# Kernel tuning notes

Measured on AMD Instinct MI355X. Metric: run time of the kernel, lower is better.

Reference implementation:

```python
import jax, jax.numpy as jnp
import numpy as np

B, S, H, NH = 4, 2048, 512, 8
HD = H // NH

def setup_inputs() -> dict:
    key = jax.random.key(0)
    ks = jax.random.split(key, 11)
    s = 1.0 / np.sqrt(H)
    return {
        "query": jax.random.normal(ks[0], (B, S, H), jnp.float32),
        "key_in": jax.random.normal(ks[1], (B, S, H), jnp.float32),
        "value": jax.random.normal(ks[2], (B, S, H), jnp.float32),
        "Wq": jax.random.uniform(ks[3], (H, H), jnp.float32, -s, s),
        "bq": jax.random.uniform(ks[4], (H,), jnp.float32, -s, s),
        "Wk": jax.random.uniform(ks[5], (H, H), jnp.float32, -s, s),
        "bk": jax.random.uniform(ks[6], (H,), jnp.float32, -s, s),
        "Wv": jax.random.uniform(ks[7], (H, H), jnp.float32, -s, s),
        "bv": jax.random.uniform(ks[8], (H,), jnp.float32, -s, s),
        "Wo": jax.random.uniform(ks[9], (H, H), jnp.float32, -s, s),
        "bo": jax.random.uniform(ks[10], (H,), jnp.float32, -s, s),
    }

def reference(query, key_in, value, Wq, bq, Wk, bk, Wv, bv, Wo, bo):
    scale = HD ** -0.5
    # projections; torch Linear: x @ W.T + b
    Q = (query @ Wq.T + bq).reshape(B, S, NH, HD).transpose(0, 2, 1, 3)   # [B,NH,S,HD]
    K = (key_in @ Wk.T + bk).reshape(B, S, NH, HD).transpose(0, 2, 1, 3)
    V = (value @ Wv.T + bv).reshape(B, S, NH, HD).transpose(0, 2, 1, 3)
    scores = jnp.einsum('bhqd,bhkd->bhqk', Q, K) * scale                  # [B,NH,S,S]
    attention = jax.nn.softmax(scores, axis=-1)                           # dropout in eval mode -> identity
    context = jnp.einsum('bhqk,bhkd->bhqd', attention, V)                 # [B,NH,S,HD]
    context = context.transpose(0, 2, 1, 3).reshape(B, S, H)
    output = context @ Wo.T + bo
    return (output, attention)
```

## Files before the change

kernel.cpp:

```cpp
#include <hip/hip_runtime.h>
#include <cstddef>

constexpr int kB  = 4;
constexpr int kS  = 2048;
constexpr int kH  = 512;
constexpr int kNH = 8;
constexpr int kHD = 64;
constexpr int kM  = kB * kS;
constexpr int kK  = 512;

#define FMA16(a, b)                                                        \
  do {                                                                     \
    acc[0][0] += a.x * b.x; acc[0][1] += a.x * b.y;                        \
    acc[0][2] += a.x * b.z; acc[0][3] += a.x * b.w;                        \
    acc[1][0] += a.y * b.x; acc[1][1] += a.y * b.y;                        \
    acc[1][2] += a.y * b.z; acc[1][3] += a.y * b.w;                        \
    acc[2][0] += a.z * b.x; acc[2][1] += a.z * b.y;                        \
    acc[2][2] += a.z * b.z; acc[2][3] += a.z * b.w;                        \
    acc[3][0] += a.w * b.x; acc[3][1] += a.w * b.y;                        \
    acc[3][2] += a.w * b.z; acc[3][3] += a.w * b.w;                        \
  } while (0)

template <int MODE>
__global__ __launch_bounds__(256) void gemm_nt_bias(
    const float* __restrict__ A, const float* __restrict__ W,
    const float* __restrict__ bias, float* __restrict__ out)
{
  __shared__ __align__(16) float As[16][68];
  __shared__ __align__(16) float Ws[16][68];

  const int tid  = threadIdx.x;
  const int ty   = tid >> 4;
  const int tx   = tid & 15;
  const int m0   = blockIdx.x * 64;
  const int n0   = blockIdx.y * 64;
  const int lrow = tid >> 2;
  const int lcol = (tid & 3) << 2;

  float acc[4][4] = {};

  for (int k0 = 0; k0 < kK; k0 += 16) {
    float4 av = *(const float4*)(A + (size_t)(m0 + lrow) * kK + k0 + lcol);
    float4 wv = *(const float4*)(W + (size_t)(n0 + lrow) * kK + k0 + lcol);
    __syncthreads();
    As[lcol + 0][lrow] = av.x; As[lcol + 1][lrow] = av.y;
    As[lcol + 2][lrow] = av.z; As[lcol + 3][lrow] = av.w;
    Ws[lcol + 0][lrow] = wv.x; Ws[lcol + 1][lrow] = wv.y;
    Ws[lcol + 2][lrow] = wv.z; Ws[lcol + 3][lrow] = wv.w;
    __syncthreads();
#pragma unroll
    for (int kk = 0; kk < 16; ++kk) {
      float4 a = *(const float4*)&As[kk][ty << 2];
      float4 b = *(const float4*)&Ws[kk][tx << 2];
      FMA16(a, b);
    }
  }

  float4 bv = *(const float4*)(bias + n0 + (tx << 2));
#pragma unroll
  for (int i = 0; i < 4; ++i) {
    const int m = m0 + (ty << 2) + i;
    float4 o = make_float4(acc[i][0] + bv.x, acc[i][1] + bv.y,
                           acc[i][2] + bv.z, acc[i][3] + bv.w);
    if (MODE == 0) {
      const int b = m >> 11;
      const int s = m & (kS - 1);
      const int h = n0 >> 6;
      const size_t idx =
          (((size_t)(b * kNH + h)) * kS + s) * kHD + (tx << 2);
      *(float4*)(out + idx) = o;
    } else {
      *(float4*)(out + (size_t)m * kH + n0 + (tx << 2)) = o;
    }
  }
}

__global__ __launch_bounds__(256) void scores_kernel(
    const float* __restrict__ Q, const float* __restrict__ Kh,
    float* __restrict__ attn)
{
  __shared__ __align__(16) float Qs[64][68];
  __shared__ __align__(16) float Ks[64][68];

  const int tid = threadIdx.x;
  const int ty  = tid >> 4;
  const int tx  = tid & 15;
  const int i0  = blockIdx.x * 64;
  const int j0  = blockIdx.y * 64;
  const int bh  = blockIdx.z;

  const float* Qb = Q  + (size_t)bh * kS * kHD;
  const float* Kb = Kh + (size_t)bh * kS * kHD;

#pragma unroll
  for (int it = 0; it < 4; ++it) {
    const int t   = tid + it * 256;
    const int row = t >> 4;
    const int c4  = (t & 15) << 2;
    float4 q  = *(const float4*)(Qb + (size_t)(i0 + row) * kHD + c4);
    float4 kv = *(const float4*)(Kb + (size_t)(j0 + row) * kHD + c4);
    Qs[c4 + 0][row] = q.x;  Qs[c4 + 1][row] = q.y;
    Qs[c4 + 2][row] = q.z;  Qs[c4 + 3][row] = q.w;
    Ks[c4 + 0][row] = kv.x; Ks[c4 + 1][row] = kv.y;
    Ks[c4 + 2][row] = kv.z; Ks[c4 + 3][row] = kv.w;
  }
  __syncthreads();

  float acc[4][4] = {};
#pragma unroll 8
  for (int kk = 0; kk < 64; ++kk) {
    float4 a = *(const float4*)&Qs[kk][ty << 2];
    float4 b = *(const float4*)&Ks[kk][tx << 2];
    FMA16(a, b);
  }

  const float scale = 0.125f;
#pragma unroll
  for (int i = 0; i < 4; ++i) {
    const size_t ridx =
        ((size_t)bh * kS + i0 + (ty << 2) + i) * kS + j0 + (tx << 2);
    *(float4*)(attn + ridx) = make_float4(acc[i][0] * scale, acc[i][1] * scale,
                                          acc[i][2] * scale, acc[i][3] * scale);
  }
}

__global__ __launch_bounds__(256) void softmax_kernel(float* __restrict__ attn)
{
  float* p = attn + (size_t)blockIdx.x * kS;
  const int tid = threadIdx.x;

  float4 v0 = ((const float4*)p)[tid];
  float4 v1 = ((const float4*)p)[tid + 256];

  float m = fmaxf(fmaxf(fmaxf(v0.x, v0.y), fmaxf(v0.z, v0.w)),
                  fmaxf(fmaxf(v1.x, v1.y), fmaxf(v1.z, v1.w)));
#pragma unroll
  for (int o = 32; o > 0; o >>= 1) m = fmaxf(m, __shfl_xor(m, o));

  __shared__ float redm[4];
  __shared__ float reds[4];
  const int w = tid >> 6;
  if ((tid & 63) == 0) redm[w] = m;
  __syncthreads();
  m = fmaxf(fmaxf(redm[0], redm[1]), fmaxf(redm[2], redm[3]));

  v0.x = __expf(v0.x - m); v0.y = __expf(v0.y - m);
  v0.z = __expf(v0.z - m); v0.w = __expf(v0.w - m);
  v1.x = __expf(v1.x - m); v1.y = __expf(v1.y - m);
  v1.z = __expf(v1.z - m); v1.w = __expf(v1.w - m);

  float s = v0.x + v0.y + v0.z + v0.w + v1.x + v1.y + v1.z + v1.w;
#pragma unroll
  for (int o = 32; o > 0; o >>= 1) s += __shfl_xor(s, o);
  if ((tid & 63) == 0) reds[w] = s;
  __syncthreads();
  s = reds[0] + reds[1] + reds[2] + reds[3];

  const float inv = 1.0f / s;
  v0.x *= inv; v0.y *= inv; v0.z *= inv; v0.w *= inv;
  v1.x *= inv; v1.y *= inv; v1.z *= inv; v1.w *= inv;
  ((float4*)p)[tid] = v0;
  ((float4*)p)[tid + 256] = v1;
}

__global__ __launch_bounds__(256) void pv_kernel(
    const float* __restrict__ attn, const float* __restrict__ V,
    float* __restrict__ ctx)
{
  __shared__ __align__(16) float Ps[64][68];
  __shared__ __align__(16) float Vs[64][68];

  const int tid = threadIdx.x;
  const int ty  = tid >> 4;
  const int tx  = tid & 15;
  const int i0  = blockIdx.x * 64;
  const int bh  = blockIdx.y;
  const int b   = bh >> 3;
  const int h   = bh & 7;

  const float* Pb = attn + ((size_t)bh * kS + i0) * kS;
  const float* Vb = V + (size_t)bh * kS * kHD;

  float acc[4][4] = {};
  for (int k0 = 0; k0 < kS; k0 += 64) {
    __syncthreads();
#pragma unroll
    for (int it = 0; it < 4; ++it) {
      const int t   = tid + it * 256;
      const int row = t >> 4;
      const int c4  = (t & 15) << 2;
      float4 pv = *(const float4*)(Pb + (size_t)row * kS + k0 + c4);
      float4 vv = *(const float4*)(Vb + (size_t)(k0 + row) * kHD + c4);
      Ps[c4 + 0][row] = pv.x; Ps[c4 + 1][row] = pv.y;
      Ps[c4 + 2][row] = pv.z; Ps[c4 + 3][row] = pv.w;
      *(float4*)&Vs[row][c4] = vv;
    }
    __syncthreads();
#pragma unroll 8
    for (int kk = 0; kk < 64; ++kk) {
      float4 a = *(const float4*)&Ps[kk][ty << 2];
      float4 b = *(const float4*)&Vs[kk][tx << 2];
      FMA16(a, b);
    }
  }

#pragma unroll
  for (int i = 0; i < 4; ++i) {
    const int s = i0 + (ty << 2) + i;
    const size_t idx = ((size_t)b * kS + s) * kH + h * kHD + (tx << 2);
    *(float4*)(ctx + idx) =
        make_float4(acc[i][0], acc[i][1], acc[i][2], acc[i][3]);
  }
}

extern "C" void kernel_launch(void* const* d_in, const int* in_sizes, int n_in,
                              void* d_out, int out_size, void* d_ws,
                              size_t ws_size, hipStream_t stream)
{
  (void)in_sizes; (void)n_in; (void)out_size;

  const float* query  = (const float*)d_in[0];
  const float* key_in = (const float*)d_in[1];
  const float* value  = (const float*)d_in[2];
  const float* Wq = (const float*)d_in[3];
  const float* bq = (const float*)d_in[4];
  const float* Wk = (const float*)d_in[5];
  const float* bk = (const float*)d_in[6];
  const float* Wv = (const float*)d_in[7];
  const float* bv = (const float*)d_in[8];
  const float* Wo = (const float*)d_in[9];
  const float* bo = (const float*)d_in[10];

  float* out  = (float*)d_out;
  float* attn = out + (size_t)kB * kS * kH;

  const size_t headElems = (size_t)kB * kNH * kS * kHD;
  if (ws_size < 4 * headElems * sizeof(float)) return;

  float* Qh  = (float*)d_ws;
  float* Kh  = Qh + headElems;
  float* Vh  = Kh + headElems;
  float* ctx = Vh + headElems;

  const dim3 blk(256);
  const dim3 gproj(kM / 64, kH / 64);
  gemm_nt_bias<0><<<gproj, blk, 0, stream>>>(query,  Wq, bq, Qh);
  gemm_nt_bias<0><<<gproj, blk, 0, stream>>>(key_in, Wk, bk, Kh);
  gemm_nt_bias<0><<<gproj, blk, 0, stream>>>(value,  Wv, bv, Vh);

  const dim3 gsc(kS / 64, kS / 64, kB * kNH);
  scores_kernel<<<gsc, blk, 0, stream>>>(Qh, Kh, attn);

  softmax_kernel<<<dim3(kB * kNH * kS), blk, 0, stream>>>(attn);

  const dim3 gpv(kS / 64, kB * kNH);
  pv_kernel<<<gpv, blk, 0, stream>>>(attn, Vh, ctx);

  gemm_nt_bias<1><<<gproj, blk, 0, stream>>>(ctx, Wo, bo, out);
}
```

Before: 1.434 ms.

## Use split-bf16 MFMA for attention scores and PV matmuls

Projections now emit Q, K and V as hi/lo bf16 pairs, with V stored transposed. The scores and PV kernels are rewritten to use 16x16x32 bf16 MFMA with three products (hi*hi, hi*lo, lo*hi) to approximate fp32 accuracy. LDS uses XOR swizzling and larger 128-row tiles. The aim is to move the dominant S×S matmuls off scalar FMA onto matrix cores, at the cost of extra conversion work, a slightly less exact result, and uncoalesced scalar stores for the transposed V and the MFMA output.

```diff
diff --git a/kernel.cpp b/kernel.cpp
--- a/kernel.cpp
+++ b/kernel.cpp
@@ -1,5 +1,6 @@
 #include <hip/hip_runtime.h>
 #include <cstddef>
+#include <cstdint>
 
 constexpr int kB  = 4;
 constexpr int kS  = 2048;
@@ -8,6 +9,24 @@
 constexpr int kHD = 64;
 constexpr int kM  = kB * kS;
 constexpr int kK  = 512;
+
+using bf16x8  = __attribute__((ext_vector_type(8))) short;
+using f32x4   = __attribute__((ext_vector_type(4))) float;
+using short4v = __attribute__((ext_vector_type(4))) short;
+
+__device__ __forceinline__ unsigned short f32_to_bf16(float f) {
+  unsigned int u = __float_as_uint(f);
+  u += 0x7FFFu + ((u >> 16) & 1u);
+  return (unsigned short)(u >> 16);
+}
+__device__ __forceinline__ float bf16_to_f32(unsigned short h) {
+  return __uint_as_float(((unsigned int)h) << 16);
+}
+__device__ __forceinline__ void split_bf16(float v, unsigned short& hi,
+                                           unsigned short& lo) {
+  hi = f32_to_bf16(v);
+  lo = f32_to_bf16(v - bf16_to_f32(hi));
+}
 
 #define FMA16(a, b)                                                        \
   do {                                                                     \
@@ -24,7 +43,8 @@
 template <int MODE>
 __global__ __launch_bounds__(256) void gemm_nt_bias(
     const float* __restrict__ A, const float* __restrict__ W,
-    const float* __restrict__ bias, float* __restrict__ out)
+    const float* __restrict__ bias, float* __restrict__ outf,
+    unsigned short* __restrict__ out_hi, unsigned short* __restrict__ out_lo)
 {
   __shared__ __align__(16) float As[16][68];
   __shared__ __align__(16) float Ws[16][68];
@@ -57,70 +77,136 @@
   }
 
   float4 bv = *(const float4*)(bias + n0 + (tx << 2));
+  const int h = n0 >> 6;
 #pragma unroll
   for (int i = 0; i < 4; ++i) {
     const int m = m0 + (ty << 2) + i;
-    float4 o = make_float4(acc[i][0] + bv.x, acc[i][1] + bv.y,
-                           acc[i][2] + bv.z, acc[i][3] + bv.w);
-    if (MODE == 0) {
+    float o[4] = {acc[i][0] + bv.x, acc[i][1] + bv.y,
+                  acc[i][2] + bv.z, acc[i][3] + bv.w};
+    if (MODE == 1) {
+      *(float4*)(outf + (size_t)m * kH + n0 + (tx << 2)) =
+          make_float4(o[0], o[1], o[2], o[3]);
+    } else {
       const int b = m >> 11;
       const int s = m & (kS - 1);
-      const int h = n0 >> 6;
-      const size_t idx =
-          (((size_t)(b * kNH + h)) * kS + s) * kHD + (tx << 2);
-      *(float4*)(out + idx) = o;
-    } else {
-      *(float4*)(out + (size_t)m * kH + n0 + (tx << 2)) = o;
-    }
-  }
-}
-
-__global__ __launch_bounds__(256) void scores_kernel(
-    const float* __restrict__ Q, const float* __restrict__ Kh,
+      const int bh = b * kNH + h;
+      unsigned short hi[4], lo[4];
+#pragma unroll
+      for (int j = 0; j < 4; ++j) split_bf16(o[j], hi[j], lo[j]);
+      if (MODE == 0) {
+        const size_t idx = (((size_t)bh) * kS + s) * kHD + (tx << 2);
+        short4v hv = {(short)hi[0], (short)hi[1], (short)hi[2], (short)hi[3]};
+        short4v lv = {(short)lo[0], (short)lo[1], (short)lo[2], (short)lo[3]};
+        *(short4v*)(out_hi + idx) = hv;
+        *(short4v*)(out_lo + idx) = lv;
+      } else {
+#pragma unroll
+        for (int j = 0; j < 4; ++j) {
+          const int d = (tx << 2) + j;
+          const size_t idx = (((size_t)bh) * kHD + d) * kS + s;
+          out_hi[idx] = hi[j];
+          out_lo[idx] = lo[j];
+        }
+      }
+    }
+  }
+}
+
+__global__ __launch_bounds__(256, 2) void scores_mfma(
+    const unsigned short* __restrict__ Qhi, const unsigned short* __restrict__ Qlo,
+    const unsigned short* __restrict__ Khi, const unsigned short* __restrict__ Klo,
     float* __restrict__ attn)
 {
-  __shared__ __align__(16) float Qs[64][68];
-  __shared__ __align__(16) float Ks[64][68];
+  __shared__ __align__(16) unsigned short lds[4 * 128 * 64];
+  unsigned short* sQh = lds;
+  unsigned short* sQl = lds + 8192;
+  unsigned short* sKh = lds + 16384;
+  unsigned short* sKl = lds + 24576;
 
   const int tid = threadIdx.x;
-  const int ty  = tid >> 4;
-  const int tx  = tid & 15;
-  const int i0  = blockIdx.x * 64;
-  const int j0  = blockIdx.y * 64;
+  const int i0  = blockIdx.x * 128;
+  const int j0  = blockIdx.y * 128;
   const int bh  = blockIdx.z;
-
-  const float* Qb = Q  + (size_t)bh * kS * kHD;
-  const float* Kb = Kh + (size_t)bh * kS * kHD;
+  const size_t hbase = (size_t)bh * kS * kHD;
+
+  const char* gq_h = (const char*)(Qhi + hbase + (size_t)i0 * kHD);
+  const char* gq_l = (const char*)(Qlo + hbase + (size_t)i0 * kHD);
+  const char* gk_h = (const char*)(Khi + hbase + (size_t)j0 * kHD);
+  const char* gk_l = (const char*)(Klo + hbase + (size_t)j0 * kHD);
 
 #pragma unroll
   for (int it = 0; it < 4; ++it) {
-    const int t   = tid + it * 256;
-    const int row = t >> 4;
-    const int c4  = (t & 15) << 2;
-    float4 q  = *(const float4*)(Qb + (size_t)(i0 + row) * kHD + c4);
-    float4 kv = *(const float4*)(Kb + (size_t)(j0 + row) * kHD + c4);
-    Qs[c4 + 0][row] = q.x;  Qs[c4 + 1][row] = q.y;
-    Qs[c4 + 2][row] = q.z;  Qs[c4 + 3][row] = q.w;
-    Ks[c4 + 0][row] = kv.x; Ks[c4 + 1][row] = kv.y;
-    Ks[c4 + 2][row] = kv.z; Ks[c4 + 3][row] = kv.w;
+    const int c   = tid + it * 256;
+    const int row = c >> 3;
+    const int bo  = (c & 7) << 4;
+    const int so  = bo ^ ((row & 7) << 4);
+    const int go  = row * 128 + bo;
+    const int lo_ = row * 128 + so;
+    *(float4*)((char*)sQh + lo_) = *(const float4*)(gq_h + go);
+    *(float4*)((char*)sQl + lo_) = *(const float4*)(gq_l + go);
+    *(float4*)((char*)sKh + lo_) = *(const float4*)(gk_h + go);
+    *(float4*)((char*)sKl + lo_) = *(const float4*)(gk_l + go);
   }
   __syncthreads();
 
-  float acc[4][4] = {};
-#pragma unroll 8
-  for (int kk = 0; kk < 64; ++kk) {
-    float4 a = *(const float4*)&Qs[kk][ty << 2];
-    float4 b = *(const float4*)&Ks[kk][tx << 2];
-    FMA16(a, b);
+  const int wid  = tid >> 6;
+  const int lane = tid & 63;
+  const int wr   = wid >> 1, wc = wid & 1;
+  const int lr   = lane & 15;
+  const int lg   = lane >> 4;
+
+  f32x4 acc[4][4];
+#pragma unroll
+  for (int m = 0; m < 4; ++m)
+#pragma unroll
+    for (int n = 0; n < 4; ++n)
+      acc[m][n] = (f32x4){0.f, 0.f, 0.f, 0.f};
+
+#pragma unroll
+  for (int ks = 0; ks < 2; ++ks) {
+    const int cb = ks * 64 + lg * 16;
+    bf16x8 aH[4], aL[4], bH[4], bL[4];
+#pragma unroll
+    for (int m = 0; m < 4; ++m) {
+      const int row = wr * 64 + m * 16 + lr;
+      const int off = row * 128 + (cb ^ ((row & 7) << 4));
+      aH[m] = *(const bf16x8*)((const char*)sQh + off);
+      aL[m] = *(const bf16x8*)((const char*)sQl + off);
+    }
+#pragma unroll
+    for (int n = 0; n < 4; ++n) {
+      const int row = wc * 64 + n * 16 + lr;
+      const int off = row * 128 + (cb ^ ((row & 7) << 4));
+      bH[n] = *(const bf16x8*)((const char*)sKh + off);
+      bL[n] = *(const bf16x8*)((const char*)sKl + off);
+    }
+#pragma unroll
+    for (int m = 0; m < 4; ++m)
+#pragma unroll
+      for (int n = 0; n < 4; ++n)
+        acc[m][n] = __builtin_amdgcn_mfma_f32_16x16x32_bf16(aH[m], bH[n], acc[m][n], 0, 0, 0);
+#pragma unroll
+    for (int m = 0; m < 4; ++m)
+#pragma unroll
+      for (int n = 0; n < 4; ++n)
+        acc[m][n] = __builtin_amdgcn_mfma_f32_16x16x32_bf16(aH[m], bL[n], acc[m][n], 0, 0, 0);
+#pragma unroll
+    for (int m = 0; m < 4; ++m)
+#pragma unroll
+      for (int n = 0; n < 4; ++n)
+        acc[m][n] = __builtin_amdgcn_mfma_f32_16x16x32_bf16(aL[m], bH[n], acc[m][n], 0, 0, 0);
   }
 
   const float scale = 0.125f;
 #pragma unroll
-  for (int i = 0; i < 4; ++i) {
-    const size_t ridx =
-        ((size_t)bh * kS + i0 + (ty << 2) + i) * kS + j0 + (tx << 2);
-    *(float4*)(attn + ridx) = make_float4(acc[i][0] * scale, acc[i][1] * scale,
-                                          acc[i][2] * scale, acc[i][3] * scale);
+  for (int m = 0; m < 4; ++m) {
+#pragma unroll
+    for (int r = 0; r < 4; ++r) {
+      const int i = i0 + wr * 64 + m * 16 + lg * 4 + r;
+      float* rowp = attn + ((size_t)bh * kS + i) * kS + j0 + wc * 64 + lr;
+#pragma unroll
+      for (int n = 0; n < 4; ++n) rowp[n * 16] = acc[m][n][r] * scale;
+    }
   }
 }
 
@@ -163,53 +249,113 @@
   ((float4*)p)[tid + 256] = v1;
 }
 
-__global__ __launch_bounds__(256) void pv_kernel(
-    const float* __restrict__ attn, const float* __restrict__ V,
+__global__ __launch_bounds__(256, 2) void pv_mfma(
+    const float* __restrict__ attn,
+    const unsigned short* __restrict__ Vthi, const unsigned short* __restrict__ Vtlo,
     float* __restrict__ ctx)
 {
-  __shared__ __align__(16) float Ps[64][68];
-  __shared__ __align__(16) float Vs[64][68];
+  __shared__ __align__(16) unsigned short sPh[128 * 64];
+  __shared__ __align__(16) unsigned short sPl[128 * 64];
+  __shared__ __align__(16) unsigned short sVh[64 * 64];
+  __shared__ __align__(16) unsigned short sVl[64 * 64];
 
   const int tid = threadIdx.x;
-  const int ty  = tid >> 4;
-  const int tx  = tid & 15;
-  const int i0  = blockIdx.x * 64;
+  const int i0  = blockIdx.x * 128;
   const int bh  = blockIdx.y;
   const int b   = bh >> 3;
   const int h   = bh & 7;
 
   const float* Pb = attn + ((size_t)bh * kS + i0) * kS;
-  const float* Vb = V + (size_t)bh * kS * kHD;
-
-  float acc[4][4] = {};
+  const unsigned short* Vh_ = Vthi + (size_t)bh * kHD * kS;
+  const unsigned short* Vl_ = Vtlo + (size_t)bh * kHD * kS;
+
+  const int wid  = tid >> 6;
+  const int lane = tid & 63;
+  const int lr   = lane & 15;
+  const int lg   = lane >> 4;
+
+  f32x4 acc[2][4];
+#pragma unroll
+  for (int m = 0; m < 2; ++m)
+#pragma unroll
+    for (int n = 0; n < 4; ++n)
+      acc[m][n] = (f32x4){0.f, 0.f, 0.f, 0.f};
+
   for (int k0 = 0; k0 < kS; k0 += 64) {
     __syncthreads();
 #pragma unroll
-    for (int it = 0; it < 4; ++it) {
-      const int t   = tid + it * 256;
-      const int row = t >> 4;
-      const int c4  = (t & 15) << 2;
-      float4 pv = *(const float4*)(Pb + (size_t)row * kS + k0 + c4);
-      float4 vv = *(const float4*)(Vb + (size_t)(k0 + row) * kHD + c4);
-      Ps[c4 + 0][row] = pv.x; Ps[c4 + 1][row] = pv.y;
-      Ps[c4 + 2][row] = pv.z; Ps[c4 + 3][row] = pv.w;
-      *(float4*)&Vs[row][c4] = vv;
+    for (int it = 0; it < 8; ++it) {
+      const int c   = tid + it * 256;
+      const int row = c >> 4;
+      const int f4  = c & 15;
+      float4 p = *(const float4*)(Pb + (size_t)row * kS + k0 + f4 * 4);
+      unsigned short h0, l0, h1, l1, h2, l2, h3, l3;
+      split_bf16(p.x, h0, l0); split_bf16(p.y, h1, l1);
+      split_bf16(p.z, h2, l2); split_bf16(p.w, h3, l3);
+      const int bo = (f4 * 8) ^ ((row & 7) << 4);
+      short4v hv = {(short)h0, (short)h1, (short)h2, (short)h3};
+      short4v lv = {(short)l0, (short)l1, (short)l2, (short)l3};
+      *(short4v*)((char*)sPh + row * 128 + bo) = hv;
+      *(short4v*)((char*)sPl + row * 128 + bo) = lv;
+    }
+#pragma unroll
+    for (int it = 0; it < 2; ++it) {
+      const int c   = tid + it * 256;
+      const int row = c >> 3;
+      const int bo  = (c & 7) << 4;
+      const int so  = bo ^ ((row & 7) << 4);
+      const char* gvh = (const char*)(Vh_ + (size_t)row * kS + k0);
+      const char* gvl = (const char*)(Vl_ + (size_t)row * kS + k0);
+      *(float4*)((char*)sVh + row * 128 + so) = *(const float4*)(gvh + bo);
+      *(float4*)((char*)sVl + row * 128 + so) = *(const float4*)(gvl + bo);
     }
     __syncthreads();
-#pragma unroll 8
-    for (int kk = 0; kk < 64; ++kk) {
-      float4 a = *(const float4*)&Ps[kk][ty << 2];
-      float4 b = *(const float4*)&Vs[kk][tx << 2];
-      FMA16(a, b);
-    }
-  }
-
-#pragma unroll
-  for (int i = 0; i < 4; ++i) {
-    const int s = i0 + (ty << 2) + i;
-    const size_t idx = ((size_t)b * kS + s) * kH + h * kHD + (tx << 2);
-    *(float4*)(ctx + idx) =
-        make_float4(acc[i][0], acc[i][1], acc[i][2], acc[i][3]);
+
+#pragma unroll
+    for (int ks = 0; ks < 2; ++ks) {
+      const int cb = ks * 64 + lg * 16;
+      bf16x8 aH[2], aL[2], bH[4], bL[4];
+#pragma unroll
+      for (int m = 0; m < 2; ++m) {
+        const int row = wid * 32 + m * 16 + lr;
+        const int off = row * 128 + (cb ^ ((row & 7) << 4));
+        aH[m] = *(const bf16x8*)((const char*)sPh + off);
+        aL[m] = *(const bf16x8*)((const char*)sPl + off);
+      }
+#pragma unroll
+      for (int n = 0; n < 4; ++n) {
+        const int row = n * 16 + lr;
+        const int off = row * 128 + (cb ^ ((row & 7) << 4));
+        bH[n] = *(const bf16x8*)((const char*)sVh + off);
+        bL[n] = *(const bf16x8*)((const char*)sVl + off);
+      }
+#pragma unroll
+      for (int m = 0; m < 2; ++m)
+#pragma unroll
+        for (int n = 0; n < 4; ++n)
+          acc[m][n] = __builtin_amdgcn_mfma_f32_16x16x32_bf16(aH[m], bH[n], acc[m][n], 0, 0, 0);
+#pragma unroll
+      for (int m = 0; m < 2; ++m)
+#pragma unroll
+        for (int n = 0; n < 4; ++n)
+          acc[m][n] = __builtin_amdgcn_mfma_f32_16x16x32_bf16(aH[m], bL[n], acc[m][n], 0, 0, 0);
+#pragma unroll
+      for (int m = 0; m < 2; ++m)
+#pragma unroll
+        for (int n = 0; n < 4; ++n)
+          acc[m][n] = __builtin_amdgcn_mfma_f32_16x16x32_bf16(aL[m], bH[n], acc[m][n], 0, 0, 0);
+    }
+  }
+
+#pragma unroll
+  for (int m = 0; m < 2; ++m) {
+#pragma unroll
+    for (int r = 0; r < 4; ++r) {
+      const int s = i0 + wid * 32 + m * 16 + lg * 4 + r;
+      float* rowp = ctx + ((size_t)b * kS + s) * kH + h * kHD + lr;
+#pragma unroll
+      for (int n = 0; n < 4; ++n) rowp[n * 16] = acc[m][n][r];
+    }
   }
 }
 
@@ -235,26 +381,29 @@
   float* attn = out + (size_t)kB * kS * kH;
 
   const size_t headElems = (size_t)kB * kNH * kS * kHD;
-  if (ws_size < 4 * headElems * sizeof(float)) return;
-
-  float* Qh  = (float*)d_ws;
-  float* Kh  = Qh + headElems;
-  float* Vh  = Kh + headElems;
-  float* ctx = Vh + headElems;
+  if (ws_size < headElems * 16) return;
+
+  unsigned short* Qhi  = (unsigned short*)d_ws;
+  unsigned short* Qlo  = Qhi + headElems;
+  unsigned short* Khi  = Qlo + headElems;
+  unsigned short* Klo  = Khi + headElems;
+  unsigned short* Vthi = Klo + headElems;
+  unsigned short* Vtlo = Vthi + headElems;
+  float* ctx = (float*)(Vtlo + headElems);
 
   const dim3 blk(256);
   const dim3 gproj(kM / 64, kH / 64);
-  gemm_nt_bias<0><<<gproj, blk, 0, stream>>>(query,  Wq, bq, Qh);
-  gemm_nt_bias<0><<<gproj, blk, 0, stream>>>(key_in, Wk, bk, Kh);
-  gemm_nt_bias<0><<<gproj, blk, 0, stream>>>(value,  Wv, bv, Vh);
-
-  const dim3 gsc(kS / 64, kS / 64, kB * kNH);
-  scores_kernel<<<gsc, blk, 0, stream>>>(Qh, Kh, attn);
+  gemm_nt_bias<0><<<gproj, blk, 0, stream>>>(query,  Wq, bq, nullptr, Qhi, Qlo);
+  gemm_nt_bias<0><<<gproj, blk, 0, stream>>>(key_in, Wk, bk, nullptr, Khi, Klo);
+  gemm_nt_bias<2><<<gproj, blk, 0, stream>>>(value,  Wv, bv, nullptr, Vthi, Vtlo);
+
+  const dim3 gsc(kS / 128, kS / 128, kB * kNH);
+  scores_mfma<<<gsc, blk, 0, stream>>>(Qhi, Qlo, Khi, Klo, attn);
 
   softmax_kernel<<<dim3(kB * kNH * kS), blk, 0, stream>>>(attn);
 
-  const dim3 gpv(kS / 64, kB * kNH);
-  pv_kernel<<<gpv, blk, 0, stream>>>(attn, Vh, ctx);
-
-  gemm_nt_bias<1><<<gproj, blk, 0, stream>>>(ctx, Wo, bo, out);
-}
+  const dim3 gpv(kS / 128, kB * kNH);
+  pv_mfma<<<gpv, blk, 0, stream>>>(attn, Vthi, Vtlo, ctx);
+
+  gemm_nt_bias<1><<<gproj, blk, 0, stream>>>(ctx, Wo, bo, out, nullptr, nullptr);
+}
```

New measurement: 1.238 ms. 1.16x faster.
